# Performance work log

Hardware: AMD Instinct MI355X
Metric: run time of the kernel (lower is better)

Reference implementation:

```python
import jax, jax.numpy as jnp
import numpy as np

G, N_REAL, C_IN, C_EDGE, H, D, C_EOUT = 4096, 31, 64, 64, 4, 64, 64
N_NODE = N_REAL + 1  # 32, last local node is the supernode


def setup_inputs() -> dict:
    key = jax.random.key(0)
    # per-graph edge template: bidirectional ring over real nodes (consecutive (u,v),(v,u) pairs),
    # then edges (u, supernode)
    u = np.arange(N_REAL)
    v = (u + 1) % N_REAL
    ring_src = np.stack([u, v], 1).reshape(-1)
    ring_dst = np.stack([v, u], 1).reshape(-1)
    ls = np.concatenate([ring_src, np.arange(N_REAL)])
    ld = np.concatenate([ring_dst, np.full(N_REAL, N_REAL)])
    Eg = ls.shape[0]  # 93
    off = np.arange(G) * N_NODE
    edge_index = np.stack([(off[:, None] + ls[None, :]).reshape(-1),
                           (off[:, None] + ld[None, :]).reshape(-1)])
    N = G * N_NODE
    E = G * Eg
    k1, k2, k3, k4, k5 = jax.random.split(key, 5)
    return {
        "x": jax.random.normal(k1, (N, C_IN), jnp.float32),
        "edge_index": jnp.asarray(edge_index, jnp.int32),
        "edge_inform": jax.random.normal(k2, (E, C_EDGE), jnp.float32) * 0.1,
        "batch": jnp.asarray(np.repeat(np.arange(G), N_NODE), jnp.int32),
        "edge_num": jnp.asarray(np.full(G, Eg), jnp.int32),
        "W_lin_l": jax.random.normal(k3, (C_IN + C_EDGE, H * D), jnp.float32) * 0.05,
        "att_l": jax.random.normal(k4, (1, H, D), jnp.float32) * 0.1,
        "bias": jnp.zeros((D,), jnp.float32),
        "W_ec": jax.random.normal(k5, (C_EDGE, C_EOUT), jnp.float32) * 0.1,
        "b_ec": jnp.zeros((C_EOUT,), jnp.float32),
    }


def reference(x, edge_index, edge_inform, batch, edge_num, W_lin_l, att_l, bias, W_ec, b_ec):
    # graph structure is static metadata -> numpy
    ei = np.asarray(edge_index)
    en = np.asarray(edge_num)
    N = x.shape[0]
    G_ = en.shape[0]
    Eg = int(en[0])
    n = N // G_
    src = jnp.asarray(ei[0])
    dst = jnp.asarray(ei[1])
    Hh, Dd = att_l.shape[1], att_l.shape[2]

    # degree counting (the per-edge python loop in the original)
    deg = jnp.zeros((N,), x.dtype).at[dst].add(1.0)

    # GAT-style edge attention + scatter-sum
    h = jnp.concatenate([x[src], edge_inform], axis=1) @ W_lin_l  # [E, H*D]
    h = h.reshape(-1, Hh, Dd)
    alpha = jax.nn.leaky_relu(jnp.sum(h * att_l, axis=-1))  # [E,H], slope 0.01
    amax = jax.ops.segment_max(alpha, dst, num_segments=N)
    ex = jnp.exp(alpha - amax[dst])
    a = ex / (jax.ops.segment_sum(ex, dst, num_segments=N)[dst] + 1e-16)
    xi = jax.ops.segment_sum(h * a[..., None], dst, num_segments=N)  # [N,H,D]
    out = xi.mean(axis=1) + bias

    # per-graph edge aggregation (structure uniform across graphs by construction)
    le = ei.reshape(2, G_, Eg) - (np.arange(G_) * n)[None, :, None]
    l0, l1 = le[0, 0], le[1, 0]  # local template indices, same for every graph
    midx = np.nonzero((l1 != n - 1) & (l0 != l1))[0]  # mask: drop supernode-dst & self-loops
    even = midx[0::2]
    C = edge_inform.shape[1]
    inf_g = edge_inform.reshape(G_, Eg, C)

    mdst = jnp.asarray(l1[midx])
    eisum = jax.vmap(lambda v: jax.ops.segment_sum(v, mdst, num_segments=n - 1))(inf_g[:, midx])  # [G,n-1,C]

    es, ed = l0[even], l1[even]
    deg_g = deg.reshape(G_, n)
    norm = deg_g[:, es] + deg_g[:, ed] - 2.0  # edge_norm; divide by edge_norm - 1
    temp = (eisum[:, es] + eisum[:, ed] - inf_g[:, even]) / (norm - 1.0)[..., None]  # [G,P,C]
    temps2 = jnp.repeat(temp, 2, axis=1)  # each temp appended twice

    l1_all = jnp.asarray(l1)
    cnt = jnp.zeros((n,), x.dtype).at[l1_all].add(1.0)
    esum_all = jax.vmap(lambda v: jax.ops.segment_sum(v, l1_all, num_segments=n))(inf_g)
    emean = esum_all / cnt[None, :, None]  # scatter reduce='mean'

    gather = jnp.concatenate([temps2, emean, emean[:, : n - 1]], axis=1).reshape(-1, C)
    new_edge_inform = jax.nn.leaky_relu(gather @ W_ec + b_ec)
    return out, new_edge_inform
```

## Files before the change

### kernel.cpp

```cpp
#include <hip/hip_runtime.h>
#include <hip/hip_fp16.h>

#define NUM_G 4096
#define RS 72
#define OUT2_OFF ((size_t)NUM_G * 32 * 64)

typedef _Float16 half8  __attribute__((ext_vector_type(8)));
typedef _Float16 half4v __attribute__((ext_vector_type(4)));
typedef float    floatx4 __attribute__((ext_vector_type(4)));

__device__ __forceinline__ float lrelu(float v) { return v > 0.f ? v : 0.01f * v; }

__global__ void setup_prep(const float* __restrict__ W, const float* __restrict__ att,
                           const float* __restrict__ Wec,
                           _Float16* __restrict__ vp16, _Float16* __restrict__ BT,
                           _Float16* __restrict__ BT2)
{
    const int t = threadIdx.x, b = blockIdx.x;
    if (b == 0) {
        for (int i = t; i < 1024; i += 256) {
            const int h8 = i >> 6, k = i & 63;
            float acc = 0.f;
            if (h8 < 8) {
                const int h = h8 & 3, ro = (h8 < 4) ? 0 : 64;
                for (int d = 0; d < 64; ++d) acc += W[(ro + k) * 256 + h * 64 + d] * att[h * 64 + d];
            }
            vp16[i] = (_Float16)acc;
        }
    }
    for (int i = b * 4096 + t; i < (b + 1) * 4096; i += 256) {
        const int d = i >> 9, kk = i & 511, h = kk >> 7, k = kk & 127;
        BT[i] = (_Float16)W[k * 256 + h * 64 + d];
    }
    for (int i = b * 512 + t; i < b * 512 + 512; i += 256) {
        const int d = i >> 6, k = i & 63;
        BT2[i] = (_Float16)Wec[k * 64 + d];
    }
}

__global__ __launch_bounds__(512, 8) void fused_main(
    const float* __restrict__ x, const float* __restrict__ einf,
    const float* __restrict__ bias, const float* __restrict__ bec,
    const _Float16* __restrict__ vp16, const _Float16* __restrict__ BT,
    const _Float16* __restrict__ BT2,
    float* __restrict__ out, float* __restrict__ out2)
{
    __shared__ __align__(16) _Float16 R[128 * RS];
    __shared__ __align__(16) _Float16 A2[64 * RS];
    __shared__ __align__(16) float    sal[128 * 9];
    __shared__ __align__(16) float    al4[93 * 4];
    __shared__ __align__(16) _Float16 virt[512];

    const int t = threadIdx.x;
    const int g = blockIdx.x;
    const int lane = t & 63;
    const int w = t >> 6;
    const int m16 = lane & 15, q = lane >> 4;

    {
        const float4* xg4 = (const float4*)(x + (size_t)g * 2048);
        {
            float4 v = xg4[t];
            half4v h4 = {(_Float16)v.x, (_Float16)v.y, (_Float16)v.z, (_Float16)v.w};
            *(half4v*)(R + (t >> 4) * RS + (t & 15) * 4) = h4;
        }
        const float4* eg4 = (const float4*)(einf + (size_t)g * 5952);
        for (int i = t; i < 1488; i += 512) {
            float4 v = eg4[i];
            half4v h4 = {(_Float16)v.x, (_Float16)v.y, (_Float16)v.z, (_Float16)v.w};
            *(half4v*)(R + (32 + (i >> 4)) * RS + (i & 15) * 4) = h4;
        }
        if (t < 27) {
            half8 z = {0, 0, 0, 0, 0, 0, 0, 0};
            *(half8*)(R + 125 * RS + t * 8) = z;
        }
    }
    __syncthreads();

    {
        const _Float16* arow = R + (w * 16 + m16) * RS;
        floatx4 s = {0.f, 0.f, 0.f, 0.f};
        #pragma unroll
        for (int kc = 0; kc < 2; ++kc) {
            half8 aF = *(const half8*)(arow + kc * 32 + q * 8);
            half8 bF = *(const half8*)(vp16 + m16 * 64 + kc * 32 + q * 8);
            s = __builtin_amdgcn_mfma_f32_16x16x32_f16(aF, bF, s, 0, 0, 0);
        }
        if (m16 < 8) {
            #pragma unroll
            for (int r = 0; r < 4; ++r)
                sal[(w * 16 + q * 4 + r) * 9 + m16] = s[r];
        }
    }
    __syncthreads();

    if (t < 128) {
        const int n = t >> 2, h = t & 3;
        if (n < 31) {
            const int s1 = (n + 30) % 31, s2 = (n + 1) % 31;
            const int e1 = 2 * s1, e2 = 2 * n + 1;
            const float a1 = lrelu(sal[s1 * 9 + h] + sal[(32 + e1) * 9 + 4 + h]);
            const float a2 = lrelu(sal[s2 * 9 + h] + sal[(32 + e2) * 9 + 4 + h]);
            const float m = fmaxf(a1, a2);
            const float x1 = __expf(a1 - m), x2 = __expf(a2 - m);
            const float inv = 1.f / (x1 + x2 + 1e-16f);
            al4[e1 * 4 + h] = x1 * inv;
            al4[e2 * 4 + h] = x2 * inv;
        } else {
            float m = -1e30f;
            for (int i = 0; i < 31; ++i)
                m = fmaxf(m, lrelu(sal[i * 9 + h] + sal[(94 + i) * 9 + 4 + h]));
            float sden = 1e-16f;
            for (int i = 0; i < 31; ++i)
                sden += __expf(lrelu(sal[i * 9 + h] + sal[(94 + i) * 9 + 4 + h]) - m);
            const float inv = 1.f / sden;
            for (int i = 0; i < 31; ++i)
                al4[(62 + i) * 4 + h] =
                    __expf(lrelu(sal[i * 9 + h] + sal[(94 + i) * 9 + 4 + h]) - m) * inv;
        }
    } else {
        const _Float16* E = R + 32 * RS;
        for (int idx = t - 128; idx < 992; idx += 384) {
            const int r = idx >> 4, c = (idx & 15) * 4;
            half4v v;
            if (r < 31) {
                const int ra = 2 * ((r + 30) % 31), rb = 2 * r + 1, rc = 2 * ((r + 1) % 31) + 1;
                v = *(const half4v*)(E + ra * RS + c) + *(const half4v*)(E + rb * RS + c)
                  + *(const half4v*)(E + rc * RS + c);
            } else {
                const int jj = r - 31;
                const int ra = 2 * ((jj + 30) % 31), rb = 2 * jj + 1;
                v = (*(const half4v*)(E + ra * RS + c) + *(const half4v*)(E + rb * RS + c))
                    * (_Float16)0.5f;
            }
            *(half4v*)(A2 + r * RS + c) = v;
        }
        if (t < 192) {
            const int c = t - 128;
            float s = 0.f;
            for (int i = 0; i < 31; ++i) s += (float)E[(62 + i) * RS + c];
            A2[62 * RS + c] = (_Float16)(s * (1.f / 31.f));
        } else if (t < 256) {
            A2[63 * RS + (t - 192)] = (_Float16)0.f;
        }
    }
    __syncthreads();

    {
        const int hf = w >> 2, nt = w & 3;
        const int base = hf ? 94 : 0;
        half8 aV, bV;
        #pragma unroll
        for (int j = 0; j < 8; ++j) {
            const int i = q * 8 + j;
            aV[j] = (m16 < 4 && i < 31) ? (_Float16)al4[(62 + i) * 4 + m16] : (_Float16)0.f;
            bV[j] = (i < 31) ? R[(base + i) * RS + nt * 16 + m16] : (_Float16)0.f;
        }
        floatx4 vc = {0.f, 0.f, 0.f, 0.f};
        vc = __builtin_amdgcn_mfma_f32_16x16x32_f16(aV, bV, vc, 0, 0, 0);
        if (q == 0) {
            #pragma unroll
            for (int r = 0; r < 4; ++r)
                virt[r * 128 + hf * 64 + nt * 16 + m16] = (_Float16)vc[r];
        }
    }
    __syncthreads();

    const int ti = w >> 2, cg = w & 3;
    const int co = cg * 16 + m16;

    {
        const int n = ti * 16 + m16;
        const int nc = (n < 31) ? n : 30;
        const int s1 = (nc + 30) % 31, s2 = (nc + 1) % 31;
        const int e1 = 2 * s1, e2 = 2 * nc + 1;
        _Float16 a1[4], a2[4];
        #pragma unroll
        for (int h = 0; h < 4; ++h) {
            a1[h] = (_Float16)al4[e1 * 4 + h];
            a2[h] = (_Float16)al4[e2 * 4 + h];
        }
        floatx4 acc = {0.f, 0.f, 0.f, 0.f};
        #pragma unroll
        for (int hf = 0; hf < 2; ++hf) {
            const int rA = hf ? 32 + e1 : s1;
            const int rB = hf ? 32 + e2 : s2;
            #pragma unroll
            for (int kc = 0; kc < 2; ++kc) {
                const int k0 = kc * 32 + q * 8;
                half8 xa = *(const half8*)(R + rA * RS + k0);
                half8 xb = *(const half8*)(R + rB * RS + k0);
                #pragma unroll
                for (int h = 0; h < 4; ++h) {
                    half8 b = *(const half8*)(BT + co * 512 + (h * 4 + hf * 2 + kc) * 32 + q * 8);
                    half8 af = xa * a1[h] + xb * a2[h];
                    if (ti == 1) {
                        half8 vv = *(const half8*)(virt + h * 128 + hf * 64 + k0);
                        af = (m16 == 15) ? vv : af;
                    }
                    acc = __builtin_amdgcn_mfma_f32_16x16x32_f16(af, b, acc, 0, 0, 0);
                }
            }
        }
        const float bv = bias[co];
        float* og = out + (size_t)g * 2048;
        #pragma unroll
        for (int r = 0; r < 4; ++r)
            og[(ti * 16 + q * 4 + r) * 64 + co] = 0.25f * acc[r] + bv;
    }

    {
        half8 b2a = *(const half8*)(BT2 + co * 64 + q * 8);
        half8 b2b = *(const half8*)(BT2 + co * 64 + 32 + q * 8);
        const int mt0 = ti * 2;
        floatx4 z = {0.f, 0.f, 0.f, 0.f};
        floatx4 acc2[2]; acc2[0] = z; acc2[1] = z;
        #pragma unroll
        for (int kk = 0; kk < 2; ++kk) {
            half8 b = kk ? b2b : b2a;
            #pragma unroll
            for (int m = 0; m < 2; ++m) {
                half8 a = *(const half8*)(A2 + ((mt0 + m) * 16 + m16) * RS + kk * 32 + q * 8);
                acc2[m] = __builtin_amdgcn_mfma_f32_16x16x32_f16(a, b, acc2[m], 0, 0, 0);
            }
        }
        const float bv2 = bec[co];
        float* o2 = out2 + (size_t)g * 8000;
        #pragma unroll
        for (int m = 0; m < 2; ++m) {
            #pragma unroll
            for (int r = 0; r < 4; ++r) {
                const int row = (mt0 + m) * 16 + q * 4 + r;
                if (row >= 63) continue;
                const float v = lrelu(acc2[m][r] + bv2);
                if (row < 31) {
                    o2[(2 * row) * 64 + co]     = v;
                    o2[(2 * row + 1) * 64 + co] = v;
                } else if (row < 62) {
                    o2[(62 + row - 31) * 64 + co] = v;
                    o2[(94 + row - 31) * 64 + co] = v;
                } else {
                    o2[93 * 64 + co] = v;
                }
            }
        }
    }
}

extern "C" void kernel_launch(void* const* d_in, const int* in_sizes, int n_in,
                              void* d_out, int out_size, void* d_ws, size_t ws_size,
                              hipStream_t stream) {
    const float* x    = (const float*)d_in[0];
    const float* einf = (const float*)d_in[2];
    const float* W    = (const float*)d_in[5];
    const float* att  = (const float*)d_in[6];
    const float* bias = (const float*)d_in[7];
    const float* Wec  = (const float*)d_in[8];
    const float* bec  = (const float*)d_in[9];
    float* out  = (float*)d_out;
    float* out2 = out + OUT2_OFF;

    _Float16* vp16 = (_Float16*)d_ws;
    _Float16* BT   = (_Float16*)((char*)d_ws + 2048);
    _Float16* BT2  = (_Float16*)((char*)d_ws + 2048 + 65536);

    setup_prep<<<8, 256, 0, stream>>>(W, att, Wec, vp16, BT, BT2);
    fused_main<<<NUM_G, 512, 0, stream>>>(x, einf, bias, bec, vp16, BT, BT2, out, out2);
}
```

Baseline: 352.2 us.

## Halve block size to 256 threads, giving each wave two output tiles

Result: faster. 323.1 us (-8.3%).

```diff
diff --git a/kernel.cpp b/kernel.cpp
--- a/kernel.cpp
+++ b/kernel.cpp
@@ -38,7 +38,7 @@
     }
 }
 
-__global__ __launch_bounds__(512, 8) void fused_main(
+__global__ __launch_bounds__(256, 4) void fused_main(
     const float* __restrict__ x, const float* __restrict__ einf,
     const float* __restrict__ bias, const float* __restrict__ bec,
     const _Float16* __restrict__ vp16, const _Float16* __restrict__ BT,
@@ -59,13 +59,13 @@
 
     {
         const float4* xg4 = (const float4*)(x + (size_t)g * 2048);
-        {
-            float4 v = xg4[t];
+        for (int i = t; i < 512; i += 256) {
+            float4 v = xg4[i];
             half4v h4 = {(_Float16)v.x, (_Float16)v.y, (_Float16)v.z, (_Float16)v.w};
-            *(half4v*)(R + (t >> 4) * RS + (t & 15) * 4) = h4;
+            *(half4v*)(R + (i >> 4) * RS + (i & 15) * 4) = h4;
         }
         const float4* eg4 = (const float4*)(einf + (size_t)g * 5952);
-        for (int i = t; i < 1488; i += 512) {
+        for (int i = t; i < 1488; i += 256) {
             float4 v = eg4[i];
             half4v h4 = {(_Float16)v.x, (_Float16)v.y, (_Float16)v.z, (_Float16)v.w};
             *(half4v*)(R + (32 + (i >> 4)) * RS + (i & 15) * 4) = h4;
@@ -75,21 +75,23 @@
             *(half8*)(R + 125 * RS + t * 8) = z;
         }
     }
-    __syncthreads();
-
-    {
-        const _Float16* arow = R + (w * 16 + m16) * RS;
+    half8 bF0 = *(const half8*)(vp16 + m16 * 64 + q * 8);
+    half8 bF1 = *(const half8*)(vp16 + m16 * 64 + 32 + q * 8);
+    __syncthreads();
+
+    #pragma unroll
+    for (int j = 0; j < 2; ++j) {
+        const int tile = w * 2 + j;
+        const _Float16* arow = R + (tile * 16 + m16) * RS;
+        half8 aF0 = *(const half8*)(arow + q * 8);
+        half8 aF1 = *(const half8*)(arow + 32 + q * 8);
         floatx4 s = {0.f, 0.f, 0.f, 0.f};
-        #pragma unroll
-        for (int kc = 0; kc < 2; ++kc) {
-            half8 aF = *(const half8*)(arow + kc * 32 + q * 8);
-            half8 bF = *(const half8*)(vp16 + m16 * 64 + kc * 32 + q * 8);
-            s = __builtin_amdgcn_mfma_f32_16x16x32_f16(aF, bF, s, 0, 0, 0);
-        }
+        s = __builtin_amdgcn_mfma_f32_16x16x32_f16(aF0, bF0, s, 0, 0, 0);
+        s = __builtin_amdgcn_mfma_f32_16x16x32_f16(aF1, bF1, s, 0, 0, 0);
         if (m16 < 8) {
             #pragma unroll
             for (int r = 0; r < 4; ++r)
-                sal[(w * 16 + q * 4 + r) * 9 + m16] = s[r];
+                sal[(tile * 16 + q * 4 + r) * 9 + m16] = s[r];
         }
     }
     __syncthreads();
@@ -120,7 +122,7 @@
         }
     } else {
         const _Float16* E = R + 32 * RS;
-        for (int idx = t - 128; idx < 992; idx += 384) {
+        for (int idx = t - 128; idx < 992; idx += 128) {
             const int r = idx >> 4, c = (idx & 15) * 4;
             half4v v;
             if (r < 31) {
@@ -140,99 +142,113 @@
             float s = 0.f;
             for (int i = 0; i < 31; ++i) s += (float)E[(62 + i) * RS + c];
             A2[62 * RS + c] = (_Float16)(s * (1.f / 31.f));
-        } else if (t < 256) {
+        } else {
             A2[63 * RS + (t - 192)] = (_Float16)0.f;
         }
     }
     __syncthreads();
 
     {
-        const int hf = w >> 2, nt = w & 3;
+        const int hf = w >> 1;
         const int base = hf ? 94 : 0;
-        half8 aV, bV;
+        half8 aV;
         #pragma unroll
         for (int j = 0; j < 8; ++j) {
             const int i = q * 8 + j;
             aV[j] = (m16 < 4 && i < 31) ? (_Float16)al4[(62 + i) * 4 + m16] : (_Float16)0.f;
-            bV[j] = (i < 31) ? R[(base + i) * RS + nt * 16 + m16] : (_Float16)0.f;
-        }
-        floatx4 vc = {0.f, 0.f, 0.f, 0.f};
-        vc = __builtin_amdgcn_mfma_f32_16x16x32_f16(aV, bV, vc, 0, 0, 0);
-        if (q == 0) {
-            #pragma unroll
-            for (int r = 0; r < 4; ++r)
-                virt[r * 128 + hf * 64 + nt * 16 + m16] = (_Float16)vc[r];
-        }
-    }
-    __syncthreads();
-
-    const int ti = w >> 2, cg = w & 3;
-    const int co = cg * 16 + m16;
-
-    {
-        const int n = ti * 16 + m16;
-        const int nc = (n < 31) ? n : 30;
-        const int s1 = (nc + 30) % 31, s2 = (nc + 1) % 31;
-        const int e1 = 2 * s1, e2 = 2 * nc + 1;
-        _Float16 a1[4], a2[4];
+        }
+        #pragma unroll
+        for (int u = 0; u < 2; ++u) {
+            const int nt = (w & 1) * 2 + u;
+            half8 bV;
+            #pragma unroll
+            for (int j = 0; j < 8; ++j) {
+                const int i = q * 8 + j;
+                bV[j] = (i < 31) ? R[(base + i) * RS + nt * 16 + m16] : (_Float16)0.f;
+            }
+            floatx4 vc = {0.f, 0.f, 0.f, 0.f};
+            vc = __builtin_amdgcn_mfma_f32_16x16x32_f16(aV, bV, vc, 0, 0, 0);
+            if (q == 0) {
+                #pragma unroll
+                for (int r = 0; r < 4; ++r)
+                    virt[r * 128 + hf * 64 + nt * 16 + m16] = (_Float16)vc[r];
+            }
+        }
+    }
+    __syncthreads();
+
+    const int co = w * 16 + m16;
+    half8 b2a = *(const half8*)(BT2 + co * 64 + q * 8);
+    half8 b2b = *(const half8*)(BT2 + co * 64 + 32 + q * 8);
+
+    {
+        const int n1c = (16 + m16 < 31) ? 16 + m16 : 30;
+        const int s1_0 = (m16 + 30) % 31, s2_0 = (m16 + 1) % 31;
+        const int e1_0 = 2 * s1_0, e2_0 = 2 * m16 + 1;
+        const int s1_1 = (n1c + 30) % 31, s2_1 = (n1c + 1) % 31;
+        const int e1_1 = 2 * s1_1, e2_1 = 2 * n1c + 1;
+        _Float16 a1_0[4], a2_0[4], a1_1[4], a2_1[4];
         #pragma unroll
         for (int h = 0; h < 4; ++h) {
-            a1[h] = (_Float16)al4[e1 * 4 + h];
-            a2[h] = (_Float16)al4[e2 * 4 + h];
-        }
-        floatx4 acc = {0.f, 0.f, 0.f, 0.f};
+            a1_0[h] = (_Float16)al4[e1_0 * 4 + h];
+            a2_0[h] = (_Float16)al4[e2_0 * 4 + h];
+            a1_1[h] = (_Float16)al4[e1_1 * 4 + h];
+            a2_1[h] = (_Float16)al4[e2_1 * 4 + h];
+        }
+        floatx4 acc0 = {0.f, 0.f, 0.f, 0.f}, acc1 = {0.f, 0.f, 0.f, 0.f};
         #pragma unroll
         for (int hf = 0; hf < 2; ++hf) {
-            const int rA = hf ? 32 + e1 : s1;
-            const int rB = hf ? 32 + e2 : s2;
+            const int rA0 = hf ? 32 + e1_0 : s1_0, rB0 = hf ? 32 + e2_0 : s2_0;
+            const int rA1 = hf ? 32 + e1_1 : s1_1, rB1 = hf ? 32 + e2_1 : s2_1;
             #pragma unroll
             for (int kc = 0; kc < 2; ++kc) {
                 const int k0 = kc * 32 + q * 8;
-                half8 xa = *(const half8*)(R + rA * RS + k0);
-                half8 xb = *(const half8*)(R + rB * RS + k0);
+                half8 x1 = *(const half8*)(R + rA0 * RS + k0);
+                half8 x2 = *(const half8*)(R + rB0 * RS + k0);
+                half8 y1 = *(const half8*)(R + rA1 * RS + k0);
+                half8 y2 = *(const half8*)(R + rB1 * RS + k0);
                 #pragma unroll
                 for (int h = 0; h < 4; ++h) {
-                    half8 b = *(const half8*)(BT + co * 512 + (h * 4 + hf * 2 + kc) * 32 + q * 8);
-                    half8 af = xa * a1[h] + xb * a2[h];
-                    if (ti == 1) {
-                        half8 vv = *(const half8*)(virt + h * 128 + hf * 64 + k0);
-                        af = (m16 == 15) ? vv : af;
-                    }
-                    acc = __builtin_amdgcn_mfma_f32_16x16x32_f16(af, b, acc, 0, 0, 0);
+                    half8 b = *(const half8*)(BT + co * 512 + h * 128 + hf * 64 + k0);
+                    half8 af0 = x1 * a1_0[h] + x2 * a2_0[h];
+                    acc0 = __builtin_amdgcn_mfma_f32_16x16x32_f16(af0, b, acc0, 0, 0, 0);
+                    half8 af1 = y1 * a1_1[h] + y2 * a2_1[h];
+                    half8 vv = *(const half8*)(virt + h * 128 + hf * 64 + k0);
+                    af1 = (m16 == 15) ? vv : af1;
+                    acc1 = __builtin_amdgcn_mfma_f32_16x16x32_f16(af1, b, acc1, 0, 0, 0);
                 }
             }
         }
         const float bv = bias[co];
         float* og = out + (size_t)g * 2048;
         #pragma unroll
-        for (int r = 0; r < 4; ++r)
-            og[(ti * 16 + q * 4 + r) * 64 + co] = 0.25f * acc[r] + bv;
-    }
-
-    {
-        half8 b2a = *(const half8*)(BT2 + co * 64 + q * 8);
-        half8 b2b = *(const half8*)(BT2 + co * 64 + 32 + q * 8);
-        const int mt0 = ti * 2;
+        for (int r = 0; r < 4; ++r) {
+            og[(q * 4 + r) * 64 + co]        = 0.25f * acc0[r] + bv;
+            og[(16 + q * 4 + r) * 64 + co]   = 0.25f * acc1[r] + bv;
+        }
+    }
+
+    {
         floatx4 z = {0.f, 0.f, 0.f, 0.f};
-        floatx4 acc2[2]; acc2[0] = z; acc2[1] = z;
+        floatx4 acc2[4]; acc2[0] = z; acc2[1] = z; acc2[2] = z; acc2[3] = z;
         #pragma unroll
         for (int kk = 0; kk < 2; ++kk) {
             half8 b = kk ? b2b : b2a;
             #pragma unroll
-            for (int m = 0; m < 2; ++m) {
-                half8 a = *(const half8*)(A2 + ((mt0 + m) * 16 + m16) * RS + kk * 32 + q * 8);
-                acc2[m] = __builtin_amdgcn_mfma_f32_16x16x32_f16(a, b, acc2[m], 0, 0, 0);
+            for (int mt = 0; mt < 4; ++mt) {
+                half8 a = *(const half8*)(A2 + (mt * 16 + m16) * RS + kk * 32 + q * 8);
+                acc2[mt] = __builtin_amdgcn_mfma_f32_16x16x32_f16(a, b, acc2[mt], 0, 0, 0);
             }
         }
         const float bv2 = bec[co];
         float* o2 = out2 + (size_t)g * 8000;
         #pragma unroll
-        for (int m = 0; m < 2; ++m) {
+        for (int mt = 0; mt < 4; ++mt) {
             #pragma unroll
             for (int r = 0; r < 4; ++r) {
-                const int row = (mt0 + m) * 16 + q * 4 + r;
+                const int row = mt * 16 + q * 4 + r;
                 if (row >= 63) continue;
-                const float v = lrelu(acc2[m][r] + bv2);
+                const float v = lrelu(acc2[mt][r] + bv2);
                 if (row < 31) {
                     o2[(2 * row) * 64 + co]     = v;
                     o2[(2 * row + 1) * 64 + co] = v;
@@ -265,5 +281,5 @@
     _Float16* BT2  = (_Float16*)((char*)d_ws + 2048 + 65536);
 
     setup_prep<<<8, 256, 0, stream>>>(W, att, Wec, vp16, BT, BT2);
-    fused_main<<<NUM_G, 512, 0, stream>>>(x, einf, bias, bec, vp16, BT, BT2, out, out2);
+    fused_main<<<NUM_G, 256, 0, stream>>>(x, einf, bias, bec, vp16, BT, BT2, out, out2);
 }
```
